# Kernel optimization log

Measured on AMD Instinct MI355X. Metric: run time of the kernel, lower is better.

## Reference

```python
import jax, jax.numpy as jnp
import numpy as np

T, B, D, H = 2048, 2, 1024, 16
DPH = D // H
SCALE = DPH ** -0.5


def setup_inputs() -> dict:
    key = jax.random.key(0)
    ks = jax.random.split(key, 5)
    x = jax.random.normal(ks[0], (T, B, D), dtype=jnp.float32)
    Wk = jax.random.normal(ks[1], (D, D), dtype=jnp.float32) * 0.02
    Wv = jax.random.normal(ks[2], (D, D), dtype=jnp.float32) * 0.02
    Wq = jax.random.normal(ks[3], (D, D), dtype=jnp.float32) * 0.02
    Wo = jax.random.normal(ks[4], (D, D), dtype=jnp.float32) * 0.02
    # causal mask: True marks positions to hide (masked_fill semantics)
    mask = jnp.triu(jnp.ones((T, T), dtype=bool), k=1)
    return {"x": x, "Wk": Wk, "Wv": Wv, "Wq": Wq, "Wo": Wo, "mask": mask}


def _split_heads(y):
    # 't b (d h) -> b h t d' : d_per_head is the OUTER factor of the split
    t, b, _ = y.shape
    return y.reshape(t, b, DPH, H).transpose(1, 3, 0, 2)  # [b, h, t, d]


def reference(x, Wk, Wv, Wq, Wo, mask):
    # nn.Linear(bias=False): y = x @ W.T
    k = _split_heads(x @ Wk.T)
    v = _split_heads(x @ Wv.T)
    q = _split_heads(x @ Wq.T)
    scores = jnp.einsum('bhid,bhjd->bhij', q, k) * SCALE  # [b,h,t,t]
    scores = jnp.where(mask, -jnp.inf, scores)
    attn = jax.nn.softmax(scores, axis=-1)
    # dropout is identity in eval mode
    out = jnp.einsum('bhij,bhjd->bhid', attn, v)  # [b,h,t,d]
    # 'b h t d -> t b (h d)' : heads are the OUTER factor of the merge
    out = out.transpose(2, 0, 1, 3).reshape(x.shape[0], x.shape[1], D)
    return out @ Wo.T
```

## Files before the change

kernel.cpp:

```cpp
#include <hip/hip_runtime.h>

#define T_LEN   2048
#define BATCH   2
#define DMODEL  1024
#define NHEAD   16
#define DHEAD   64
#define MROWS   4096
#define KDIM    1024
#define NDIM    1024
#define ATT_SC2 (0.125f * 1.44269504088896f)

typedef unsigned short u16;
typedef unsigned int   u32;
typedef u16   u16x8 __attribute__((ext_vector_type(8)));
typedef u16   u16x4 __attribute__((ext_vector_type(4)));
typedef __bf16 bf16x8 __attribute__((ext_vector_type(8)));
typedef float f32x4 __attribute__((ext_vector_type(4)));

__device__ __forceinline__ u16 f2bf(float f) {
  u32 u = __builtin_bit_cast(u32, f);
  u += 0x7fffu + ((u >> 16) & 1u);
  return (u16)(u >> 16);
}

__device__ __forceinline__ u16 bfc(float f) {
  return __builtin_bit_cast(u16, (__bf16)f);
}

__device__ __forceinline__ f32x4 mfma16(u16x8 a, u16x8 b, f32x4 c) {
  return __builtin_amdgcn_mfma_f32_16x16x32_bf16(
      __builtin_bit_cast(bf16x8, a), __builtin_bit_cast(bf16x8, b), c, 0, 0, 0);
}

__device__ __forceinline__ void gload16(const u16* g, u16* l) {
  __builtin_amdgcn_global_load_lds((const __attribute__((address_space(1))) void*)g,
                                   (__attribute__((address_space(3))) void*)l,
                                   16, 0, 0);
}

#define XN 4194304u
__global__ __launch_bounds__(256) void cast_all(
    const float* __restrict__ x,  const float* __restrict__ wk,
    const float* __restrict__ wv, const float* __restrict__ wq,
    const float* __restrict__ wo, u16* __restrict__ ws) {
  size_t i = ((size_t)blockIdx.x * 256 + threadIdx.x) * 4;
  const float* src; size_t soff, doff; float sc = 1.0f;
  if (i < XN) {
    int m = (int)(i >> 10), d = (int)(i & 1023);
    int t = m >> 1, b = m & 1;
    src = x; soff = i;
    doff = ((size_t)(b * 2048 + t) << 10) + d;
  } else {
    size_t off = i - XN;
    int wi = (int)(off >> 20);
    off &= 1048575u;
    int u = (int)(off >> 10), c = (int)(off & 1023);
    src = (wi == 0) ? wk : (wi == 1) ? wv : (wi == 2) ? wq : wo;
    soff = off;
    if (wi == 3) {
      doff = XN + 3u * 1048576u + off;
    } else {
      int slot = (wi == 2) ? 0 : (wi == 0) ? 1 : 2;
      int up = (u & 15) * 64 + (u >> 4);
      doff = XN + (size_t)slot * 1048576u + ((size_t)up << 10) + c;
      if (wi == 2) sc = ATT_SC2;
    }
  }
  float4 v = *reinterpret_cast<const float4*>(src + soff);
  u16x4 o;
  o.s0 = f2bf(v.x * sc); o.s1 = f2bf(v.y * sc); o.s2 = f2bf(v.z * sc); o.s3 = f2bf(v.w * sc);
  *reinterpret_cast<u16x4*>(ws + doff) = o;
}

__global__ __launch_bounds__(256, 2) void gemm_qkv(
    const u16* __restrict__ xbm, const u16* __restrict__ Wqkv,
    u16* __restrict__ Qh, u16* __restrict__ Kh, u16* __restrict__ Vt) {
  __shared__ __align__(16) u16 As[256 * 64];
  __shared__ __align__(16) u16 Bs[128 * 64];

  const int tid = threadIdx.x;
  const int l  = tid & 63, w = tid >> 6;
  const int lr = l & 15,  lg = l >> 4;
  const int wm = w >> 1,  wn = w & 1;

  const int blk  = blockIdx.x;
  const int wgid = (blk & 7) * 48 + (blk >> 3);

  const u16 *A, *W;
  int m0, n0, isV;
  if (wgid < 256) {
    const int bx = wgid >> 4, by = wgid & 15;
    A = xbm; W = Wqkv; m0 = by * 256; n0 = bx * 128; isV = 0;
  } else {
    const int v = wgid - 256;
    const int vby = v >> 5, vbx = v & 31;
    A = Wqkv + (2048u << 10); W = xbm; m0 = vby * 256; n0 = vbx * 128; isV = 1;
  }

  f32x4 acc[8][4];
#pragma unroll
  for (int i = 0; i < 8; ++i)
#pragma unroll
    for (int j = 0; j < 4; ++j) acc[i][j] = (f32x4)(0.0f);

  for (int k0 = 0; k0 < KDIM; k0 += 64) {
#pragma unroll
    for (int i = 0; i < 8; ++i) {
      const int base = i * 256 + w * 64;
      const int p = base + l;
      const int r = p >> 3, c = p & 7;
      gload16(A + (size_t)(m0 + r) * KDIM + k0 + ((c ^ (r & 7)) << 3),
              As + (size_t)base * 8);
    }
#pragma unroll
    for (int i = 0; i < 4; ++i) {
      const int base = i * 256 + w * 64;
      const int p = base + l;
      const int r = p >> 3, c = p & 7;
      gload16(W + (size_t)(n0 + r) * KDIM + k0 + ((c ^ (r & 7)) << 3),
              Bs + (size_t)base * 8);
    }
    __syncthreads();

#pragma unroll
    for (int ks = 0; ks < 2; ++ks) {
      const int cr = ks * 4 + lg;
      u16x8 bf_[4];
#pragma unroll
      for (int ni = 0; ni < 4; ++ni) {
        const int rr = wn * 64 + ni * 16 + lr;
        bf_[ni] = *reinterpret_cast<const u16x8*>(Bs + rr * 64 + ((cr ^ (rr & 7)) << 3));
      }
      __builtin_amdgcn_s_setprio(1);
#pragma unroll
      for (int mi = 0; mi < 8; ++mi) {
        const int rr = wm * 128 + mi * 16 + lr;
        const u16x8 af = *reinterpret_cast<const u16x8*>(
            As + rr * 64 + ((cr ^ (rr & 7)) << 3));
#pragma unroll
        for (int ni = 0; ni < 4; ++ni)
          acc[mi][ni] = mfma16(af, bf_[ni], acc[mi][ni]);
      }
      __builtin_amdgcn_s_setprio(0);
    }
    __syncthreads();
  }

#pragma unroll
  for (int mi = 0; mi < 8; ++mi)
#pragma unroll
    for (int ni = 0; ni < 4; ++ni)
#pragma unroll
      for (int r = 0; r < 4; ++r) {
        const int row = m0 + wm * 128 + mi * 16 + lg * 4 + r;
        const int col = n0 + wn * 64 + ni * 16 + lr;
        const u16 v = bfc(acc[mi][ni][r]);
        if (!isV) {
          const int bb = row >> 11, t = row & 2047;
          const int c = col & 1023, hh = c >> 6, dp = c & 63;
          u16* d = (col < 1024) ? Qh : Kh;
          d[(((size_t)(bb * NHEAD + hh) << 11) + t) * 64 + dp] = v;
        } else {
          const int hh = row >> 6, dp = row & 63;
          const int bb = col >> 11, t = col & 2047;
          Vt[((((size_t)(bb * NHEAD + hh)) * 64 + dp) << 11) + t] = v;
        }
      }
}

__global__ __launch_bounds__(256) void gemm_o(
    const u16* __restrict__ A, const u16* __restrict__ W, float* __restrict__ out) {
  __shared__ __align__(16) u16 As[128 * 64];
  __shared__ __align__(16) u16 Bs[128 * 64];

  const int tid = threadIdx.x;
  const int l  = tid & 63, w = tid >> 6;
  const int lr = l & 15,  lg = l >> 4;
  const int wm = w >> 1,  wn = w & 1;
  const int m0 = blockIdx.y * 128;
  const int n0 = blockIdx.x * 128;

  f32x4 acc[4][4];
#pragma unroll
  for (int i = 0; i < 4; ++i)
#pragma unroll
    for (int j = 0; j < 4; ++j) acc[i][j] = (f32x4)(0.0f);

  for (int k0 = 0; k0 < KDIM; k0 += 64) {
#pragma unroll
    for (int i = 0; i < 4; ++i) {
      int p  = i * 256 + tid;
      int r  = p >> 3, cph = p & 7;
      int cl = cph ^ (r & 7);
      u16* ldsA = As + (size_t)(i * 256 + w * 64) * 8;
      u16* ldsB = Bs + (size_t)(i * 256 + w * 64) * 8;
      gload16(A + (size_t)(m0 + r) * KDIM + k0 + cl * 8, ldsA);
      gload16(W + (size_t)(n0 + r) * KDIM + k0 + cl * 8, ldsB);
    }
    __syncthreads();

#pragma unroll
    for (int ks = 0; ks < 2; ++ks) {
      u16x8 af[4], bf_[4];
      const int cr = ks * 4 + lg;
#pragma unroll
      for (int mi = 0; mi < 4; ++mi) {
        int rr = wm * 64 + mi * 16 + lr;
        af[mi] = *reinterpret_cast<const u16x8*>(As + rr * 64 + ((cr ^ (rr & 7)) * 8));
      }
#pragma unroll
      for (int ni = 0; ni < 4; ++ni) {
        int rr = wn * 64 + ni * 16 + lr;
        bf_[ni] = *reinterpret_cast<const u16x8*>(Bs + rr * 64 + ((cr ^ (rr & 7)) * 8));
      }
#pragma unroll
      for (int mi = 0; mi < 4; ++mi)
#pragma unroll
        for (int ni = 0; ni < 4; ++ni)
          acc[mi][ni] = mfma16(af[mi], bf_[ni], acc[mi][ni]);
    }
    __syncthreads();
  }

#pragma unroll
  for (int mi = 0; mi < 4; ++mi)
#pragma unroll
    for (int ni = 0; ni < 4; ++ni)
#pragma unroll
      for (int r = 0; r < 4; ++r) {
        int row = m0 + wm * 64 + mi * 16 + lg * 4 + r;
        int col = n0 + wn * 64 + ni * 16 + lr;
        int t = row & 2047, bb = row >> 11;
        out[((size_t)(t * 2 + bb) << 10) + col] = acc[mi][ni][r];
      }
}

__global__ __launch_bounds__(256) void attn_fwd(
    const u16* __restrict__ Qh, const u16* __restrict__ Kh,
    const u16* __restrict__ Vt, u16* __restrict__ Aout) {
  __shared__ __align__(16) u16 Ks[2][8192];
  __shared__ __align__(16) u16 Vs[2][8192];
  __shared__ __align__(16) u16 Pl[4][1024];

  const int tid = threadIdx.x;
  const int l = tid & 63, w = tid >> 6;
  const int lr = l & 15, lg = l >> 4;
  const int blk = blockIdx.x;
  const int bxx = (blk >> 3) & 15;
  const int bh  = ((blk >> 7) << 3) + (blk & 7);
  const int b = bh >> 4, h = bh & 15;

  const u16* kg = Kh + ((size_t)bh << 17);
  const u16* vg = Vt + ((size_t)bh << 17);

  const u16x8 ones = {0x3F80,0x3F80,0x3F80,0x3F80,0x3F80,0x3F80,0x3F80,0x3F80};

  auto stage = [&](int buf, int kv0) {
#pragma unroll
    for (int j = 0; j < 4; ++j) {
      const int base = (j * 4 + w) * 64;
      const int g = base + l;
      const int rk = g >> 3, ck = g & 7;
      gload16(kg + (size_t)(kv0 + rk) * 64 + ((ck ^ (rk & 7)) << 3),
              &Ks[buf][(size_t)base * 8]);
      const int rv = g >> 4, cv = g & 15;
      gload16(vg + ((size_t)rv << 11) + kv0 + ((cv ^ (rv & 15)) << 3),
              &Vs[buf][(size_t)base * 8]);
    }
  };

  for (int ph = 0; ph < 2; ++ph) {
    const int qb = ph ? bxx : 31 - bxx;
    const int qbase = qb * 64 + w * 16;
    const int qrow = qbase + lr;

    const u16* qptr = Qh + (((size_t)bh << 11) + qrow) * 64 + lg * 8;
    const u16x8 qf0 = *reinterpret_cast<const u16x8*>(qptr);
    const u16x8 qf1 = *reinterpret_cast<const u16x8*>(qptr + 32);

    f32x4 oacc[4];
#pragma unroll
    for (int i = 0; i < 4; ++i) oacc[i] = (f32x4)(0.0f);
    f32x4 sum4 = (f32x4)(0.0f);
    float m_ = -1e30f;

    const int npair = (qb + 2) >> 1;
    stage(0, 0);
    __syncthreads();

    int cur = 0;
    for (int t = 0; t < npair; ++t) {
      const int kv0 = t * 128;
      if (t + 1 < npair) stage(cur ^ 1, kv0 + 128);

      float p[2][4][4];
      __builtin_amdgcn_s_setprio(1);
#pragma unroll
      for (int hh = 0; hh < 2; ++hh) {
        const int i64 = 2 * t + hh;
        if (i64 <= qb) {
#pragma unroll
          for (int tt = 0; tt < 4; ++tt) {
            const int row = hh * 64 + tt * 16 + lr;
            const u16x8 kf0 = *reinterpret_cast<const u16x8*>(
                &Ks[cur][row * 64 + ((lg ^ (row & 7)) << 3)]);
            const u16x8 kf1 = *reinterpret_cast<const u16x8*>(
                &Ks[cur][row * 64 + (((4 + lg) ^ (row & 7)) << 3)]);
            f32x4 sacc = (f32x4)(0.0f);
            sacc = mfma16(kf0, qf0, sacc);
            sacc = mfma16(kf1, qf1, sacc);
#pragma unroll
            for (int r = 0; r < 4; ++r) p[hh][tt][r] = sacc[r];
          }
          if (i64 == qb) {
#pragma unroll
            for (int tt = 0; tt < 4; ++tt)
#pragma unroll
              for (int r = 0; r < 4; ++r) {
                const int kv = kv0 + hh * 64 + tt * 16 + lg * 4 + r;
                if (kv > qrow) p[hh][tt][r] = -1e30f;
              }
          }
        } else {
#pragma unroll
          for (int tt = 0; tt < 4; ++tt)
#pragma unroll
            for (int r = 0; r < 4; ++r) p[hh][tt][r] = -1e30f;
        }
      }
      __builtin_amdgcn_s_setprio(0);

      float mx = p[0][0][0];
#pragma unroll
      for (int hh = 0; hh < 2; ++hh)
#pragma unroll
        for (int tt = 0; tt < 4; ++tt)
#pragma unroll
          for (int r = 0; r < 4; ++r) mx = fmaxf(mx, p[hh][tt][r]);
      mx = fmaxf(mx, __shfl_xor(mx, 16, 64));
      mx = fmaxf(mx, __shfl_xor(mx, 32, 64));

      if (__any(mx > m_ + 8.0f)) {
        const float mnew = fmaxf(m_, mx);
        const float al = __builtin_amdgcn_exp2f(m_ - mnew);
        m_ = mnew;
#pragma unroll
        for (int r = 0; r < 4; ++r) {
          const float ab = __shfl(al, lg * 4 + r, 64);
          sum4[r] *= ab;
          oacc[0][r] *= ab; oacc[1][r] *= ab; oacc[2][r] *= ab; oacc[3][r] *= ab;
        }
      }

#pragma unroll
      for (int hh = 0; hh < 2; ++hh)
#pragma unroll
        for (int tt = 0; tt < 4; ++tt)
#pragma unroll
          for (int r = 0; r < 4; ++r)
            p[hh][tt][r] = __builtin_amdgcn_exp2f(p[hh][tt][r] - m_);

#pragma unroll
      for (int kvh = 0; kvh < 2; ++kvh) {
#pragma unroll
        for (int tt = 0; tt < 4; ++tt) {
          u16x4 pk;
          pk.s0 = bfc(p[kvh][tt][0]); pk.s1 = bfc(p[kvh][tt][1]);
          pk.s2 = bfc(p[kvh][tt][2]); pk.s3 = bfc(p[kvh][tt][3]);
          *reinterpret_cast<u16x4*>(
              &Pl[w][lr * 64 + (((tt * 2 + (lg >> 1)) ^ (lr & 7)) << 3)
                     + ((lg & 1) << 2)]) = pk;
        }
        __builtin_amdgcn_s_setprio(1);
#pragma unroll
        for (int kh = 0; kh < 2; ++kh) {
          const u16x8 pa = *reinterpret_cast<const u16x8*>(
              &Pl[w][lr * 64 + (((kh * 4 + lg) ^ (lr & 7)) << 3)]);
          sum4 = mfma16(pa, ones, sum4);
#pragma unroll
          for (int ni = 0; ni < 4; ++ni) {
            const int dr = ni * 16 + lr;
            const int ck = kvh * 8 + kh * 4 + lg;
            const u16x8 vf = *reinterpret_cast<const u16x8*>(
                &Vs[cur][dr * 128 + ((ck ^ (dr & 15)) << 3)]);
            oacc[ni] = mfma16(pa, vf, oacc[ni]);
          }
        }
        __builtin_amdgcn_s_setprio(0);
      }

      __syncthreads();
      cur ^= 1;
    }

#pragma unroll
    for (int r = 0; r < 4; ++r) {
      const float inv = 1.0f / sum4[r];
      const int q = qbase + lg * 4 + r;
      const size_t rowbase = (((size_t)(b * 2048 + q)) << 10) + h * DHEAD;
#pragma unroll
      for (int ni = 0; ni < 4; ++ni)
        Aout[rowbase + ni * 16 + lr] = bfc(oacc[ni][r] * inv);
    }
  }
}

extern "C" void kernel_launch(void* const* d_in, const int* in_sizes, int n_in,
                              void* d_out, int out_size, void* d_ws, size_t ws_size,
                              hipStream_t stream) {
  const float* x  = (const float*)d_in[0];
  const float* Wk = (const float*)d_in[1];
  const float* Wv = (const float*)d_in[2];
  const float* Wq = (const float*)d_in[3];
  const float* Wo = (const float*)d_in[4];

  u16* ws   = (u16*)d_ws;
  u16* xbm  = ws;
  u16* Wqkv = xbm + 4194304;
  u16* Wob  = Wqkv + 3145728;
  u16* Qh   = Wob + 1048576;
  u16* Kh   = Qh  + 4194304;
  u16* Vt   = Kh  + 4194304;
  u16* Aout = Vt  + 4194304;

  cast_all<<<8192, 256, 0, stream>>>(x, Wk, Wv, Wq, Wo, ws);

  gemm_qkv<<<384, 256, 0, stream>>>(xbm, Wqkv, Qh, Kh, Vt);

  attn_fwd<<<512, 256, 0, stream>>>(Qh, Kh, Vt, Aout);

  gemm_o<<<dim3(8, 32), 256, 0, stream>>>(Aout, Wob, (float*)d_out);
}
```

Baseline: 113.3 us.

## Split attention into one query tile per block with 64-wide KV tiles

The attention kernel now launches twice as many blocks, each handling a single 64-row query tile instead of a paired short/long tile. KV staging tiles shrink from 128 to 64 keys, which halves LDS use and removes the wasted half-tile of masked work on the diagonal. A new block-to-(head, query-tile) mapping interleaves short and long causal tiles across XCDs to balance load. The cost is more blocks, more reloading of K/V per head, and less work per block to hide latency behind.

Result: slower. 118.0 us (+4.1%).

```diff
diff --git a/kernel.cpp b/kernel.cpp
--- a/kernel.cpp
+++ b/kernel.cpp
@@ -238,16 +238,20 @@
 __global__ __launch_bounds__(256) void attn_fwd(
     const u16* __restrict__ Qh, const u16* __restrict__ Kh,
     const u16* __restrict__ Vt, u16* __restrict__ Aout) {
-  __shared__ __align__(16) u16 Ks[2][8192];
-  __shared__ __align__(16) u16 Vs[2][8192];
+  __shared__ __align__(16) u16 Ks[2][4096];
+  __shared__ __align__(16) u16 Vs[2][4096];
   __shared__ __align__(16) u16 Pl[4][1024];
 
   const int tid = threadIdx.x;
   const int l = tid & 63, w = tid >> 6;
   const int lr = l & 15, lg = l >> 4;
   const int blk = blockIdx.x;
-  const int bxx = (blk >> 3) & 15;
-  const int bh  = ((blk >> 7) << 3) + (blk & 7);
+  const int xcd = blk & 7;
+  const int idx = blk >> 3;
+  const int g = idx >> 2, m = idx & 3;
+  const int bh = xcd + 8 * m;
+  const int gg = (m & 2) ? ((g + 16) & 31) : g;
+  const int qb = (m & 1) ? (31 - gg) : gg;
   const int b = bh >> 4, h = bh & 15;
 
   const u16* kg = Kh + ((size_t)bh << 17);
@@ -257,151 +261,128 @@
 
   auto stage = [&](int buf, int kv0) {
 #pragma unroll
-    for (int j = 0; j < 4; ++j) {
+    for (int j = 0; j < 2; ++j) {
       const int base = (j * 4 + w) * 64;
-      const int g = base + l;
-      const int rk = g >> 3, ck = g & 7;
-      gload16(kg + (size_t)(kv0 + rk) * 64 + ((ck ^ (rk & 7)) << 3),
-              &Ks[buf][(size_t)base * 8]);
-      const int rv = g >> 4, cv = g & 15;
-      gload16(vg + ((size_t)rv << 11) + kv0 + ((cv ^ (rv & 15)) << 3),
-              &Vs[buf][(size_t)base * 8]);
+      const int p = base + l;
+      const int r = p >> 3, c = p & 7;
+      const int cs = ((c ^ (r & 7)) << 3);
+      gload16(kg + (size_t)(kv0 + r) * 64 + cs, &Ks[buf][(size_t)base * 8]);
+      gload16(vg + ((size_t)r << 11) + kv0 + cs, &Vs[buf][(size_t)base * 8]);
     }
   };
 
-  for (int ph = 0; ph < 2; ++ph) {
-    const int qb = ph ? bxx : 31 - bxx;
-    const int qbase = qb * 64 + w * 16;
-    const int qrow = qbase + lr;
-
-    const u16* qptr = Qh + (((size_t)bh << 11) + qrow) * 64 + lg * 8;
-    const u16x8 qf0 = *reinterpret_cast<const u16x8*>(qptr);
-    const u16x8 qf1 = *reinterpret_cast<const u16x8*>(qptr + 32);
-
-    f32x4 oacc[4];
-#pragma unroll
-    for (int i = 0; i < 4; ++i) oacc[i] = (f32x4)(0.0f);
-    f32x4 sum4 = (f32x4)(0.0f);
-    float m_ = -1e30f;
-
-    const int npair = (qb + 2) >> 1;
-    stage(0, 0);
+  const int qbase = qb * 64 + w * 16;
+  const int qrow = qbase + lr;
+
+  const u16* qptr = Qh + (((size_t)bh << 11) + qrow) * 64 + lg * 8;
+  const u16x8 qf0 = *reinterpret_cast<const u16x8*>(qptr);
+  const u16x8 qf1 = *reinterpret_cast<const u16x8*>(qptr + 32);
+
+  f32x4 oacc[4];
+#pragma unroll
+  for (int i = 0; i < 4; ++i) oacc[i] = (f32x4)(0.0f);
+  f32x4 sum4 = (f32x4)(0.0f);
+  float m_ = -1e30f;
+
+  const int nt = qb + 1;
+  stage(0, 0);
+  __syncthreads();
+
+  int cur = 0;
+  for (int t = 0; t < nt; ++t) {
+    const int kv0 = t * 64;
+    if (t + 1 < nt) stage(cur ^ 1, kv0 + 64);
+
+    float p[4][4];
+    __builtin_amdgcn_s_setprio(1);
+#pragma unroll
+    for (int tt = 0; tt < 4; ++tt) {
+      const int row = tt * 16 + lr;
+      const u16x8 kf0 = *reinterpret_cast<const u16x8*>(
+          &Ks[cur][row * 64 + ((lg ^ (row & 7)) << 3)]);
+      const u16x8 kf1 = *reinterpret_cast<const u16x8*>(
+          &Ks[cur][row * 64 + (((4 + lg) ^ (row & 7)) << 3)]);
+      f32x4 sacc = (f32x4)(0.0f);
+      sacc = mfma16(kf0, qf0, sacc);
+      sacc = mfma16(kf1, qf1, sacc);
+#pragma unroll
+      for (int r = 0; r < 4; ++r) p[tt][r] = sacc[r];
+    }
+    __builtin_amdgcn_s_setprio(0);
+    if (t == nt - 1) {
+#pragma unroll
+      for (int tt = 0; tt < 4; ++tt)
+#pragma unroll
+        for (int r = 0; r < 4; ++r) {
+          const int kv = kv0 + tt * 16 + lg * 4 + r;
+          if (kv > qrow) p[tt][r] = -1e30f;
+        }
+    }
+
+    float mx = p[0][0];
+#pragma unroll
+    for (int tt = 0; tt < 4; ++tt)
+#pragma unroll
+      for (int r = 0; r < 4; ++r) mx = fmaxf(mx, p[tt][r]);
+    mx = fmaxf(mx, __shfl_xor(mx, 16, 64));
+    mx = fmaxf(mx, __shfl_xor(mx, 32, 64));
+
+    if (__any(mx > m_ + 8.0f)) {
+      const float mnew = fmaxf(m_, mx);
+      const float al = __builtin_amdgcn_exp2f(m_ - mnew);
+      m_ = mnew;
+#pragma unroll
+      for (int r = 0; r < 4; ++r) {
+        const float ab = __shfl(al, lg * 4 + r, 64);
+        sum4[r] *= ab;
+        oacc[0][r] *= ab; oacc[1][r] *= ab; oacc[2][r] *= ab; oacc[3][r] *= ab;
+      }
+    }
+
+#pragma unroll
+    for (int tt = 0; tt < 4; ++tt)
+#pragma unroll
+      for (int r = 0; r < 4; ++r)
+        p[tt][r] = __builtin_amdgcn_exp2f(p[tt][r] - m_);
+
+#pragma unroll
+    for (int tt = 0; tt < 4; ++tt) {
+      u16x4 pk;
+      pk.s0 = bfc(p[tt][0]); pk.s1 = bfc(p[tt][1]);
+      pk.s2 = bfc(p[tt][2]); pk.s3 = bfc(p[tt][3]);
+      *reinterpret_cast<u16x4*>(
+          &Pl[w][lr * 64 + (((tt * 2 + (lg >> 1)) ^ (lr & 7)) << 3)
+                 + ((lg & 1) << 2)]) = pk;
+    }
+
+    __builtin_amdgcn_s_setprio(1);
+#pragma unroll
+    for (int kh = 0; kh < 2; ++kh) {
+      const u16x8 pa = *reinterpret_cast<const u16x8*>(
+          &Pl[w][lr * 64 + (((kh * 4 + lg) ^ (lr & 7)) << 3)]);
+      sum4 = mfma16(pa, ones, sum4);
+#pragma unroll
+      for (int ni = 0; ni < 4; ++ni) {
+        const int dr = ni * 16 + lr;
+        const u16x8 vf = *reinterpret_cast<const u16x8*>(
+            &Vs[cur][dr * 64 + (((kh * 4 + lg) ^ (dr & 7)) << 3)]);
+        oacc[ni] = mfma16(pa, vf, oacc[ni]);
+      }
+    }
+    __builtin_amdgcn_s_setprio(0);
+
     __syncthreads();
-
-    int cur = 0;
-    for (int t = 0; t < npair; ++t) {
-      const int kv0 = t * 128;
-      if (t + 1 < npair) stage(cur ^ 1, kv0 + 128);
-
-      float p[2][4][4];
-      __builtin_amdgcn_s_setprio(1);
-#pragma unroll
-      for (int hh = 0; hh < 2; ++hh) {
-        const int i64 = 2 * t + hh;
-        if (i64 <= qb) {
-#pragma unroll
-          for (int tt = 0; tt < 4; ++tt) {
-            const int row = hh * 64 + tt * 16 + lr;
-            const u16x8 kf0 = *reinterpret_cast<const u16x8*>(
-                &Ks[cur][row * 64 + ((lg ^ (row & 7)) << 3)]);
-            const u16x8 kf1 = *reinterpret_cast<const u16x8*>(
-                &Ks[cur][row * 64 + (((4 + lg) ^ (row & 7)) << 3)]);
-            f32x4 sacc = (f32x4)(0.0f);
-            sacc = mfma16(kf0, qf0, sacc);
-            sacc = mfma16(kf1, qf1, sacc);
-#pragma unroll
-            for (int r = 0; r < 4; ++r) p[hh][tt][r] = sacc[r];
-          }
-          if (i64 == qb) {
-#pragma unroll
-            for (int tt = 0; tt < 4; ++tt)
-#pragma unroll
-              for (int r = 0; r < 4; ++r) {
-                const int kv = kv0 + hh * 64 + tt * 16 + lg * 4 + r;
-                if (kv > qrow) p[hh][tt][r] = -1e30f;
-              }
-          }
-        } else {
-#pragma unroll
-          for (int tt = 0; tt < 4; ++tt)
-#pragma unroll
-            for (int r = 0; r < 4; ++r) p[hh][tt][r] = -1e30f;
-        }
-      }
-      __builtin_amdgcn_s_setprio(0);
-
-      float mx = p[0][0][0];
-#pragma unroll
-      for (int hh = 0; hh < 2; ++hh)
-#pragma unroll
-        for (int tt = 0; tt < 4; ++tt)
-#pragma unroll
-          for (int r = 0; r < 4; ++r) mx = fmaxf(mx, p[hh][tt][r]);
-      mx = fmaxf(mx, __shfl_xor(mx, 16, 64));
-      mx = fmaxf(mx, __shfl_xor(mx, 32, 64));
-
-      if (__any(mx > m_ + 8.0f)) {
-        const float mnew = fmaxf(m_, mx);
-        const float al = __builtin_amdgcn_exp2f(m_ - mnew);
-        m_ = mnew;
-#pragma unroll
-        for (int r = 0; r < 4; ++r) {
-          const float ab = __shfl(al, lg * 4 + r, 64);
-          sum4[r] *= ab;
-          oacc[0][r] *= ab; oacc[1][r] *= ab; oacc[2][r] *= ab; oacc[3][r] *= ab;
-        }
-      }
-
-#pragma unroll
-      for (int hh = 0; hh < 2; ++hh)
-#pragma unroll
-        for (int tt = 0; tt < 4; ++tt)
-#pragma unroll
-          for (int r = 0; r < 4; ++r)
-            p[hh][tt][r] = __builtin_amdgcn_exp2f(p[hh][tt][r] - m_);
-
-#pragma unroll
-      for (int kvh = 0; kvh < 2; ++kvh) {
-#pragma unroll
-        for (int tt = 0; tt < 4; ++tt) {
-          u16x4 pk;
-          pk.s0 = bfc(p[kvh][tt][0]); pk.s1 = bfc(p[kvh][tt][1]);
-          pk.s2 = bfc(p[kvh][tt][2]); pk.s3 = bfc(p[kvh][tt][3]);
-          *reinterpret_cast<u16x4*>(
-              &Pl[w][lr * 64 + (((tt * 2 + (lg >> 1)) ^ (lr & 7)) << 3)
-                     + ((lg & 1) << 2)]) = pk;
-        }
-        __builtin_amdgcn_s_setprio(1);
-#pragma unroll
-        for (int kh = 0; kh < 2; ++kh) {
-          const u16x8 pa = *reinterpret_cast<const u16x8*>(
-              &Pl[w][lr * 64 + (((kh * 4 + lg) ^ (lr & 7)) << 3)]);
-          sum4 = mfma16(pa, ones, sum4);
-#pragma unroll
-          for (int ni = 0; ni < 4; ++ni) {
-            const int dr = ni * 16 + lr;
-            const int ck = kvh * 8 + kh * 4 + lg;
-            const u16x8 vf = *reinterpret_cast<const u16x8*>(
-                &Vs[cur][dr * 128 + ((ck ^ (dr & 15)) << 3)]);
-            oacc[ni] = mfma16(pa, vf, oacc[ni]);
-          }
-        }
-        __builtin_amdgcn_s_setprio(0);
-      }
-
-      __syncthreads();
-      cur ^= 1;
-    }
-
-#pragma unroll
-    for (int r = 0; r < 4; ++r) {
-      const float inv = 1.0f / sum4[r];
-      const int q = qbase + lg * 4 + r;
-      const size_t rowbase = (((size_t)(b * 2048 + q)) << 10) + h * DHEAD;
-#pragma unroll
-      for (int ni = 0; ni < 4; ++ni)
-        Aout[rowbase + ni * 16 + lr] = bfc(oacc[ni][r] * inv);
-    }
+    cur ^= 1;
+  }
+
+#pragma unroll
+  for (int r = 0; r < 4; ++r) {
+    const float inv = 1.0f / sum4[r];
+    const int q = qbase + lg * 4 + r;
+    const size_t rowbase = (((size_t)(b * 2048 + q)) << 10) + h * DHEAD;
+#pragma unroll
+    for (int ni = 0; ni < 4; ++ni)
+      Aout[rowbase + ni * 16 + lr] = bfc(oacc[ni][r] * inv);
   }
 }
 
@@ -427,7 +408,7 @@
 
   gemm_qkv<<<384, 256, 0, stream>>>(xbm, Wqkv, Qh, Kh, Vt);
 
-  attn_fwd<<<512, 256, 0, stream>>>(Qh, Kh, Vt, Aout);
+  attn_fwd<<<1024, 256, 0, stream>>>(Qh, Kh, Vt, Aout);
 
   gemm_o<<<dim3(8, 32), 256, 0, stream>>>(Aout, Wob, (float*)d_out);
 }
```
